# Kernel optimization log

Hardware: AMD Instinct MI355X
Metric: run time of the kernel (lower is better)

The kernel has to match this reference:

```python
import jax, jax.numpy as jnp
import numpy as np

N, T, D, K = 32, 8192, 64, 64
LOG2PI = float(np.log(2.0 * np.pi))


def setup_inputs() -> dict:
    key = jax.random.key(0)
    k1, k2, k3, k4 = jax.random.split(key, 4)
    x = jax.random.normal(k1, (N, T, D), dtype=jnp.float32)
    # valid GMM params: positive weights summing to 1, positive diagonal covariances
    weights = jax.nn.softmax(jax.random.normal(k2, (K,), dtype=jnp.float32))
    means = jax.random.normal(k3, (K, D), dtype=jnp.float32)
    covars = jax.random.uniform(k4, (K, D), dtype=jnp.float32, minval=0.5, maxval=1.5)
    return {"x": x, "weights": weights, "means": means, "covars": covars}


def _posterior(x, weights, means, covars):
    # diagonal-GMM predict_proba without materializing [N,T,K,D]:
    # sum_d (x-mu)^2/c = sum x^2/c - 2 sum x*mu/c + sum mu^2/c
    inv_c = 1.0 / covars                                   # [K,D]
    quad = (jnp.einsum('ntd,kd->ntk', x * x, inv_c)
            - 2.0 * jnp.einsum('ntd,kd->ntk', x, means * inv_c)
            + jnp.sum(means * means * inv_c, axis=-1))      # [N,T,K]
    log_prob = (jnp.log(weights)
                - 0.5 * (D * LOG2PI + jnp.sum(jnp.log(covars), axis=-1) + quad))
    return jax.nn.softmax(log_prob, axis=-1)               # [N,T,K]


def reference(x, weights, means, covars):
    # p = predict_proba * weights, renormalized over K (as in the torch code)
    p = _posterior(x, weights, means, covars) * weights
    p = p / jnp.sum(p, axis=-1, keepdims=True)             # [N,T,K]

    # pooled statistics over T (einsum avoids the [N,T,K,D] intermediate)
    s0 = jnp.sum(p, axis=1)                                # [N,K]
    s1 = jnp.einsum('ntk,ntd->nkd', p, x)                  # [N,K,D]
    s2 = jnp.einsum('ntk,ntd->nkd', p, x * x)              # [N,K,D]

    sw = jnp.sqrt(weights)                                 # [K]
    v0 = (s0 - T * weights) / sw                           # [N,K]
    v1 = (s1 - means * s0[..., None]) / (sw[:, None] * jnp.sqrt(covars))
    v2 = (s2 - 2.0 * means * s1 + (means ** 2 - covars) * s0[..., None]) / (
        jnp.sqrt(jnp.float32(2.0)) * sw[:, None] * covars)

    v = jnp.concatenate([v0[..., None], v1, v2], axis=2).reshape(x.shape[0], -1)
    # power normalization then L2 normalization
    v = jnp.sign(v) * jnp.sqrt(jnp.abs(v))
    v = v / jnp.linalg.norm(v, axis=1, keepdims=True)
    return v
```

## Files before the change

kernel.cpp:

```cpp
#include <hip/hip_runtime.h>
#include <math.h>

#define N_  32
#define T_  8192
#define D_  64
#define K_  64
#define CHUNKS 32
#define TOK_PER_BLOCK (T_ / CHUNKS)
#define TB 64
#define NBATCH (TOK_PER_BLOCK / TB)
#define STATS_PER_N (K_ + 2 * K_ * D_)
#define XSTR 72

typedef _Float16 half_t;
typedef __attribute__((ext_vector_type(8)))  _Float16 v8h;
typedef __attribute__((ext_vector_type(4)))  float    v4f;
typedef __attribute__((ext_vector_type(16))) float    v16f;

__global__ void prep_kernel(const float* __restrict__ w, const float* __restrict__ mu,
                            const float* __restrict__ cv, float* __restrict__ Ap,
                            half_t* __restrict__ WH, float* __restrict__ ssq) {
    if (blockIdx.x < 8) {
#pragma unroll
        for (int i = 0; i < 4; ++i) {
            const int e = blockIdx.x * 1024 + i * 256 + threadIdx.x;
            const int j = e & 7, l = (e >> 3) & 63, fs = e >> 9;
            const int tile = fs >> 2, s = fs & 3;
            const int kc = 16 * tile + (l & 15);
            const int f  = 32 * s + 8 * (l >> 4) + j;
            float val;
            if (f < 64) val = mu[kc * 64 + f] / cv[kc * 64 + f];
            else        val = -0.5f / cv[kc * 64 + (f - 64)];
            WH[e] = (half_t)val;
        }
    } else {
        if (threadIdx.x < 32) ssq[threadIdx.x] = 0.f;
        if (threadIdx.x < K_) {
            const int k = threadIdx.x;
            float acc = 0.f;
            for (int d = 0; d < D_; ++d) {
                const int idx = k * D_ + d;
                const float c = cv[idx], m = mu[idx];
                acc += logf(c) + m * m / c;
            }
            Ap[k] = 2.f * logf(w[k]) - 0.5f * acc;
        }
    }
}

__launch_bounds__(256, 3)
__global__ void main_kernel(const float* __restrict__ x, const float* __restrict__ Ap,
                            const half_t* __restrict__ WH, float* __restrict__ outbuf,
                            int mode) {
    __shared__ half_t Xs[TB][XSTR];
    __shared__ half_t Qs[TB][XSTR];
    __shared__ half_t Pt[K_][XSTR];
    __shared__ float  s0sh[4][64];

    const int tid  = threadIdx.x;
    const int lane = tid & 63;
    const int wv   = tid >> 6;
    const int chunk = blockIdx.x;
    const int n     = blockIdx.y;
    const int q     = lane >> 4;
    const int c0    = lane & 15;
    const int tok   = 16 * wv + c0;

    v8h Wf[16];
#pragma unroll
    for (int t = 0; t < 4; ++t)
#pragma unroll
        for (int s = 0; s < 4; ++s)
            Wf[t * 4 + s] = *(const v8h*)(WH + (size_t)((t * 4 + s) * 64 + lane) * 8);

    float apv[16];
#pragma unroll
    for (int t = 0; t < 4; ++t)
#pragma unroll
        for (int r = 0; r < 4; ++r) apv[t * 4 + r] = Ap[16 * t + 4 * q + r];

    float S0loc[16];
#pragma unroll
    for (int j = 0; j < 16; ++j) S0loc[j] = 0.f;

    const int sig = wv >> 1;
    const int dh  = wv & 1;
    v16f accB[2];
#pragma unroll
    for (int m = 0; m < 2; ++m)
#pragma unroll
        for (int r = 0; r < 16; ++r) accB[m][r] = 0.f;

    const size_t xbase = ((size_t)n * T_ + (size_t)chunk * TOK_PER_BLOCK) * (size_t)D_;
    const float* xrow0 = x + xbase + tok * 64 + 8 * q;

    float4 R[4];
    R[0] = *(const float4*)(xrow0);
    R[1] = *(const float4*)(xrow0 + 4);
    R[2] = *(const float4*)(xrow0 + 32);
    R[3] = *(const float4*)(xrow0 + 36);

#pragma unroll 1
    for (int batch = 0; batch < NBATCH; ++batch) {
        v8h xh0, xh1, qh0, qh1;
        {
            const float4 a = R[0], b = R[1], c = R[2], d = R[3];
            xh0[0] = (half_t)a.x; xh0[1] = (half_t)a.y; xh0[2] = (half_t)a.z; xh0[3] = (half_t)a.w;
            xh0[4] = (half_t)b.x; xh0[5] = (half_t)b.y; xh0[6] = (half_t)b.z; xh0[7] = (half_t)b.w;
            xh1[0] = (half_t)c.x; xh1[1] = (half_t)c.y; xh1[2] = (half_t)c.z; xh1[3] = (half_t)c.w;
            xh1[4] = (half_t)d.x; xh1[5] = (half_t)d.y; xh1[6] = (half_t)d.z; xh1[7] = (half_t)d.w;
            qh0[0] = (half_t)(a.x * a.x); qh0[1] = (half_t)(a.y * a.y);
            qh0[2] = (half_t)(a.z * a.z); qh0[3] = (half_t)(a.w * a.w);
            qh0[4] = (half_t)(b.x * b.x); qh0[5] = (half_t)(b.y * b.y);
            qh0[6] = (half_t)(b.z * b.z); qh0[7] = (half_t)(b.w * b.w);
            qh1[0] = (half_t)(c.x * c.x); qh1[1] = (half_t)(c.y * c.y);
            qh1[2] = (half_t)(c.z * c.z); qh1[3] = (half_t)(c.w * c.w);
            qh1[4] = (half_t)(d.x * d.x); qh1[5] = (half_t)(d.y * d.y);
            qh1[6] = (half_t)(d.z * d.z); qh1[7] = (half_t)(d.w * d.w);
            *(v8h*)&Xs[tok][8 * q]      = xh0;
            *(v8h*)&Xs[tok][32 + 8 * q] = xh1;
            *(v8h*)&Qs[tok][8 * q]      = qh0;
            *(v8h*)&Qs[tok][32 + 8 * q] = qh1;
        }

        if (batch + 1 < NBATCH) {
            const float* xr = xrow0 + (size_t)(batch + 1) * TB * D_;
            R[0] = *(const float4*)(xr);
            R[1] = *(const float4*)(xr + 4);
            R[2] = *(const float4*)(xr + 32);
            R[3] = *(const float4*)(xr + 36);
        }

        {
            v4f acc[4];
#pragma unroll
            for (int t = 0; t < 4; ++t) acc[t] = (v4f)(0.f);
#pragma unroll
            for (int t = 0; t < 4; ++t) {
                acc[t] = __builtin_amdgcn_mfma_f32_16x16x32_f16(Wf[t * 4 + 0], xh0, acc[t], 0, 0, 0);
                acc[t] = __builtin_amdgcn_mfma_f32_16x16x32_f16(Wf[t * 4 + 1], xh1, acc[t], 0, 0, 0);
                acc[t] = __builtin_amdgcn_mfma_f32_16x16x32_f16(Wf[t * 4 + 2], qh0, acc[t], 0, 0, 0);
                acc[t] = __builtin_amdgcn_mfma_f32_16x16x32_f16(Wf[t * 4 + 3], qh1, acc[t], 0, 0, 0);
            }
            float pv[16];
            float m = -1e30f;
#pragma unroll
            for (int t = 0; t < 4; ++t)
#pragma unroll
                for (int r = 0; r < 4; ++r) {
                    const float lg = acc[t][r] + apv[t * 4 + r];
                    pv[t * 4 + r] = lg;
                    m = fmaxf(m, lg);
                }
            m = fmaxf(m, __shfl_xor(m, 16, 64));
            m = fmaxf(m, __shfl_xor(m, 32, 64));
            float ssum = 0.f;
#pragma unroll
            for (int j = 0; j < 16; ++j) { pv[j] = __expf(pv[j] - m); ssum += pv[j]; }
            ssum += __shfl_xor(ssum, 16, 64);
            ssum += __shfl_xor(ssum, 32, 64);
            const float rs = 1.f / ssum;
#pragma unroll
            for (int j = 0; j < 16; ++j) { pv[j] *= rs; S0loc[j] += pv[j]; }
#pragma unroll
            for (int t = 0; t < 4; ++t)
#pragma unroll
                for (int r = 0; r < 4; ++r)
                    Pt[16 * t + 4 * q + r][tok] = (half_t)pv[t * 4 + r];
        }
        __syncthreads();

        {
            const half_t* Bsrc = (sig == 0) ? &Xs[0][0] : &Qs[0][0];
            const int m   = lane & 31;
            const int h   = lane >> 5;
            const int d   = 32 * dh + m;
            const half_t* Arow0 = &Pt[m][0];
            const half_t* Arow1 = &Pt[32 + m][0];
#pragma unroll
            for (int st = 0; st < 4; ++st) {
                const int tB = 16 * st + 8 * h;
                const v8h a0 = *(const v8h*)(Arow0 + tB);
                const v8h a1 = *(const v8h*)(Arow1 + tB);
                v8h bf;
#pragma unroll
                for (int j = 0; j < 8; ++j)
                    bf[j] = Bsrc[(tB + j) * XSTR + d];
                accB[0] = __builtin_amdgcn_mfma_f32_32x32x16_f16(a0, bf, accB[0], 0, 0, 0);
                accB[1] = __builtin_amdgcn_mfma_f32_32x32x16_f16(a1, bf, accB[1], 0, 0, 0);
            }
        }
        __syncthreads();
    }

#pragma unroll
    for (int j = 0; j < 16; ++j) {
        float v = S0loc[j];
        v += __shfl_xor(v, 1, 64);
        v += __shfl_xor(v, 2, 64);
        v += __shfl_xor(v, 4, 64);
        v += __shfl_xor(v, 8, 64);
        S0loc[j] = v;
    }
    if (c0 == 0) {
#pragma unroll
        for (int t = 0; t < 4; ++t)
#pragma unroll
            for (int r = 0; r < 4; ++r)
                s0sh[wv][16 * t + 4 * q + r] = S0loc[t * 4 + r];
    }
    __syncthreads();

    if (mode == 1) {
        float* dstb = outbuf + (size_t)(n * CHUNKS + chunk) * STATS_PER_N;
        if (tid < 64)
            dstb[tid] = s0sh[0][tid] + s0sh[1][tid] + s0sh[2][tid] + s0sh[3][tid];
        const int d = 32 * dh + (lane & 31);
        float* dst = dstb + 64 + sig * 4096;
#pragma unroll
        for (int mt = 0; mt < 2; ++mt)
#pragma unroll
            for (int r = 0; r < 16; ++r) {
                const int kc = 32 * mt + (r & 3) + 8 * (r >> 2) + 4 * (lane >> 5);
                dst[kc * 64 + d] = accB[mt][r];
            }
    } else {
        float* sb = outbuf + (size_t)n * STATS_PER_N;
        if (tid < 64)
            atomicAdd(&sb[tid], s0sh[0][tid] + s0sh[1][tid] + s0sh[2][tid] + s0sh[3][tid]);
        const int d = 32 * dh + (lane & 31);
        float* dst = sb + 64 + sig * 4096;
#pragma unroll
        for (int mt = 0; mt < 2; ++mt)
#pragma unroll
            for (int r = 0; r < 16; ++r) {
                const int kc = 32 * mt + (r & 3) + 8 * (r >> 2) + 4 * (lane >> 5);
                atomicAdd(&dst[kc * 64 + d], accB[mt][r]);
            }
    }
}

__global__ void reduce_pow_kernel(const float* __restrict__ partials,
                                  const float* __restrict__ w, const float* __restrict__ mu,
                                  const float* __restrict__ cv,
                                  float* __restrict__ us, float* __restrict__ ssq) {
    __shared__ float red[4];
    const int e = blockIdx.x * 256 + threadIdx.x;
    const int n = blockIdx.y;
    float u = 0.f;
    if (e < STATS_PER_N) {
        const float* base = partials + (size_t)n * CHUNKS * STATS_PER_N;
        float sv = 0.f;
#pragma unroll 8
        for (int c = 0; c < CHUNKS; ++c) sv += base[(size_t)c * STATS_PER_N + e];
        float v; int oidx;
        if (e < 64) {
            const float wv = w[e];
            v = (sv - (float)T_ * wv) * rsqrtf(wv);
            oidx = e * 129;
        } else if (e < 64 + 4096) {
            const int idx = e - 64, k = idx >> 6, d = idx & 63;
            float s0v = 0.f;
#pragma unroll 8
            for (int c = 0; c < CHUNKS; ++c) s0v += base[(size_t)c * STATS_PER_N + k];
            v = (sv - mu[idx] * s0v) * rsqrtf(w[k] * cv[idx]);
            oidx = k * 129 + 1 + d;
        } else {
            const int idx = e - 4160, k = idx >> 6, d = idx & 63;
            float s0v = 0.f, s1v = 0.f;
#pragma unroll 4
            for (int c = 0; c < CHUNKS; ++c) {
                s0v += base[(size_t)c * STATS_PER_N + k];
                s1v += base[(size_t)c * STATS_PER_N + 64 + idx];
            }
            const float m_ = mu[idx], c_ = cv[idx];
            v = (sv - 2.f * m_ * s1v + (m_ * m_ - c_) * s0v) * (rsqrtf(2.f * w[k]) / c_);
            oidx = k * 129 + 65 + d;
        }
        u = (v >= 0.f) ? sqrtf(v) : -sqrtf(-v);
        us[(size_t)n * STATS_PER_N + oidx] = u;
    }
    float ss = u * u;
#pragma unroll
    for (int off = 32; off > 0; off >>= 1) ss += __shfl_xor(ss, off, 64);
    if ((threadIdx.x & 63) == 0) red[threadIdx.x >> 6] = ss;
    __syncthreads();
    if (threadIdx.x == 0)
        atomicAdd(&ssq[n], red[0] + red[1] + red[2] + red[3]);
}

__global__ void scale_kernel(const float* __restrict__ us, const float* __restrict__ ssq,
                             float* __restrict__ out) {
    const int e = blockIdx.x * 256 + threadIdx.x;
    const int n = blockIdx.y;
    if (e < STATS_PER_N)
        out[(size_t)n * STATS_PER_N + e] = us[(size_t)n * STATS_PER_N + e] * rsqrtf(ssq[n]);
}

__global__ void fin_kernel(const float* __restrict__ w, const float* __restrict__ mu,
                           const float* __restrict__ cv, const float* __restrict__ stats,
                           float* __restrict__ out) {
    __shared__ float us[STATS_PER_N];
    __shared__ float red[4];
    const int n   = blockIdx.x;
    const int tid = threadIdx.x;
    const float* sb = stats + (size_t)n * STATS_PER_N;

    float ss = 0.f;
    if (tid < 64) {
        const float wv = w[tid];
        const float v = (sb[tid] - (float)T_ * wv) * rsqrtf(wv);
        const float u = (v >= 0.f) ? sqrtf(v) : -sqrtf(-v);
        us[tid * 129] = u;
        ss = fmaf(u, u, ss);
    }
#pragma unroll 1
    for (int i = 0; i < 16; ++i) {
        const int idx = i * 256 + tid;
        const int k = idx >> 6, d = idx & 63;
        const float v = (sb[64 + idx] - mu[idx] * sb[k]) * rsqrtf(w[k] * cv[idx]);
        const float u = (v >= 0.f) ? sqrtf(v) : -sqrtf(-v);
        us[k * 129 + 1 + d] = u;
        ss = fmaf(u, u, ss);
    }
#pragma unroll 1
    for (int i = 0; i < 16; ++i) {
        const int idx = i * 256 + tid;
        const int k = idx >> 6, d = idx & 63;
        const float m_ = mu[idx], c_ = cv[idx];
        const float s1v = sb[64 + idx], s2v = sb[64 + 4096 + idx];
        const float v = (s2v - 2.f * m_ * s1v + (m_ * m_ - c_) * sb[k]) *
                        (rsqrtf(2.f * w[k]) / c_);
        const float u = (v >= 0.f) ? sqrtf(v) : -sqrtf(-v);
        us[k * 129 + 65 + d] = u;
        ss = fmaf(u, u, ss);
    }
#pragma unroll
    for (int off = 32; off > 0; off >>= 1) ss += __shfl_xor(ss, off, 64);
    if ((tid & 63) == 0) red[tid >> 6] = ss;
    __syncthreads();
    const float tot = red[0] + red[1] + red[2] + red[3];
    const float rn = rsqrtf(tot);
    for (int e = tid; e < STATS_PER_N; e += 256)
        out[(size_t)n * STATS_PER_N + e] = us[e] * rn;
}

extern "C" void kernel_launch(void* const* d_in, const int* in_sizes, int n_in,
                              void* d_out, int out_size, void* d_ws, size_t ws_size,
                              hipStream_t stream) {
    const float* x  = (const float*)d_in[0];
    const float* w  = (const float*)d_in[1];
    const float* mu = (const float*)d_in[2];
    const float* cv = (const float*)d_in[3];
    float* out = (float*)d_out;

    const size_t part_elems = (size_t)CHUNKS * N_ * STATS_PER_N;
    const size_t us_elems   = (size_t)N_ * STATS_PER_N;
    const size_t need_big = (part_elems + us_elems + 32 + K_ + (size_t)K_ * 64) * sizeof(float);

    if (ws_size >= need_big) {
        float* partials = (float*)d_ws;
        float* us  = partials + part_elems;
        float* ssq = us + us_elems;
        float* Ap  = ssq + 32;
        half_t* WH = (half_t*)(Ap + K_);

        prep_kernel<<<9, 256, 0, stream>>>(w, mu, cv, Ap, WH, ssq);
        main_kernel<<<dim3(CHUNKS, N_), 256, 0, stream>>>(x, Ap, WH, partials, 1);
        reduce_pow_kernel<<<dim3(33, N_), 256, 0, stream>>>(partials, w, mu, cv, us, ssq);
        scale_kernel<<<dim3(33, N_), 256, 0, stream>>>(us, ssq, out);
    } else {
        float* stats = (float*)d_ws;
        float* ssq = stats + us_elems;
        float* Ap  = ssq + 32;
        half_t* WH = (half_t*)(Ap + K_);

        hipMemsetAsync(stats, 0, us_elems * sizeof(float), stream);
        prep_kernel<<<9, 256, 0, stream>>>(w, mu, cv, Ap, WH, ssq);
        main_kernel<<<dim3(CHUNKS, N_), 256, 0, stream>>>(x, Ap, WH, stats, 0);
        fin_kernel<<<N_, 256, 0, stream>>>(w, mu, cv, stats, out);
    }
}
```

Measured before the change: 154.6 us.

## Process 128-token batches per block with 16 chunks and two token groups

Halves the number of chunks per sequence so each block covers 512 tokens, and doubles the batch to 128 tokens by having each wave process two 16-token groups before each barrier pair. The goal is to cut the number of __syncthreads per token, the number of partial-stat blocks that must be reduced afterwards, and to double register prefetch depth. In exchange it uses more shared memory and registers (launch bounds drop to 2 blocks per CU) and launches fewer blocks, which may reduce occupancy and latency hiding.

```diff
diff --git a/kernel.cpp b/kernel.cpp
--- a/kernel.cpp
+++ b/kernel.cpp
@@ -5,12 +5,12 @@
 #define T_  8192
 #define D_  64
 #define K_  64
-#define CHUNKS 32
-#define TOK_PER_BLOCK (T_ / CHUNKS)
-#define TB 64
-#define NBATCH (TOK_PER_BLOCK / TB)
+#define CHUNKS 16
+#define TB 128
+#define NBATCH 4
 #define STATS_PER_N (K_ + 2 * K_ * D_)
 #define XSTR 72
+#define PSTR 136
 
 typedef _Float16 half_t;
 typedef __attribute__((ext_vector_type(8)))  _Float16 v8h;
@@ -48,13 +48,13 @@
     }
 }
 
-__launch_bounds__(256, 3)
+__launch_bounds__(256, 2)
 __global__ void main_kernel(const float* __restrict__ x, const float* __restrict__ Ap,
                             const half_t* __restrict__ WH, float* __restrict__ outbuf,
                             int mode) {
     __shared__ half_t Xs[TB][XSTR];
     __shared__ half_t Qs[TB][XSTR];
-    __shared__ half_t Pt[K_][XSTR];
+    __shared__ half_t Pt[K_][PSTR];
     __shared__ float  s0sh[4][64];
 
     const int tid  = threadIdx.x;
@@ -64,7 +64,8 @@
     const int n     = blockIdx.y;
     const int q     = lane >> 4;
     const int c0    = lane & 15;
-    const int tok   = 16 * wv + c0;
+    const int tok0  = 16 * wv + c0;
+    const int tok1  = tok0 + 64;
 
     v8h Wf[16];
 #pragma unroll
@@ -91,83 +92,88 @@
 #pragma unroll
         for (int r = 0; r < 16; ++r) accB[m][r] = 0.f;
 
-    const size_t xbase = ((size_t)n * T_ + (size_t)chunk * TOK_PER_BLOCK) * (size_t)D_;
-    const float* xrow0 = x + xbase + tok * 64 + 8 * q;
-
-    float4 R[4];
-    R[0] = *(const float4*)(xrow0);
-    R[1] = *(const float4*)(xrow0 + 4);
-    R[2] = *(const float4*)(xrow0 + 32);
-    R[3] = *(const float4*)(xrow0 + 36);
+    const size_t xbase = ((size_t)n * T_ + (size_t)chunk * (NBATCH * TB)) * (size_t)D_;
+    const float* xrow0 = x + xbase + tok0 * 64 + 8 * q;
+    const float* xrow1 = x + xbase + tok1 * 64 + 8 * q;
+
+    float4 RA[4], RB[4];
+    RA[0] = *(const float4*)(xrow0);      RA[1] = *(const float4*)(xrow0 + 4);
+    RA[2] = *(const float4*)(xrow0 + 32); RA[3] = *(const float4*)(xrow0 + 36);
+    RB[0] = *(const float4*)(xrow1);      RB[1] = *(const float4*)(xrow1 + 4);
+    RB[2] = *(const float4*)(xrow1 + 32); RB[3] = *(const float4*)(xrow1 + 36);
+
+#define PROCESS_GROUP(Rg, xrowg, tokg)                                          \
+    {                                                                           \
+        v8h xh0, xh1, qh0, qh1;                                                 \
+        {                                                                       \
+            const float4 a = Rg[0], b = Rg[1], c = Rg[2], d = Rg[3];            \
+            xh0[0] = (half_t)a.x; xh0[1] = (half_t)a.y; xh0[2] = (half_t)a.z; xh0[3] = (half_t)a.w; \
+            xh0[4] = (half_t)b.x; xh0[5] = (half_t)b.y; xh0[6] = (half_t)b.z; xh0[7] = (half_t)b.w; \
+            xh1[0] = (half_t)c.x; xh1[1] = (half_t)c.y; xh1[2] = (half_t)c.z; xh1[3] = (half_t)c.w; \
+            xh1[4] = (half_t)d.x; xh1[5] = (half_t)d.y; xh1[6] = (half_t)d.z; xh1[7] = (half_t)d.w; \
+            qh0[0] = (half_t)(a.x * a.x); qh0[1] = (half_t)(a.y * a.y);         \
+            qh0[2] = (half_t)(a.z * a.z); qh0[3] = (half_t)(a.w * a.w);         \
+            qh0[4] = (half_t)(b.x * b.x); qh0[5] = (half_t)(b.y * b.y);         \
+            qh0[6] = (half_t)(b.z * b.z); qh0[7] = (half_t)(b.w * b.w);         \
+            qh1[0] = (half_t)(c.x * c.x); qh1[1] = (half_t)(c.y * c.y);         \
+            qh1[2] = (half_t)(c.z * c.z); qh1[3] = (half_t)(c.w * c.w);         \
+            qh1[4] = (half_t)(d.x * d.x); qh1[5] = (half_t)(d.y * d.y);         \
+            qh1[6] = (half_t)(d.z * d.z); qh1[7] = (half_t)(d.w * d.w);         \
+            *(v8h*)&Xs[tokg][8 * q]      = xh0;                                 \
+            *(v8h*)&Xs[tokg][32 + 8 * q] = xh1;                                 \
+            *(v8h*)&Qs[tokg][8 * q]      = qh0;                                 \
+            *(v8h*)&Qs[tokg][32 + 8 * q] = qh1;                                 \
+        }                                                                       \
+        if (batch + 1 < NBATCH) {                                               \
+            const float* xr = xrowg + (size_t)(batch + 1) * TB * D_;            \
+            Rg[0] = *(const float4*)(xr);                                       \
+            Rg[1] = *(const float4*)(xr + 4);                                   \
+            Rg[2] = *(const float4*)(xr + 32);                                  \
+            Rg[3] = *(const float4*)(xr + 36);                                  \
+        }                                                                       \
+        {                                                                       \
+            v4f acc[4];                                                         \
+            _Pragma("unroll")                                                   \
+            for (int t = 0; t < 4; ++t) acc[t] = (v4f)(0.f);                    \
+            _Pragma("unroll")                                                   \
+            for (int t = 0; t < 4; ++t) {                                       \
+                acc[t] = __builtin_amdgcn_mfma_f32_16x16x32_f16(Wf[t * 4 + 0], xh0, acc[t], 0, 0, 0); \
+                acc[t] = __builtin_amdgcn_mfma_f32_16x16x32_f16(Wf[t * 4 + 1], xh1, acc[t], 0, 0, 0); \
+                acc[t] = __builtin_amdgcn_mfma_f32_16x16x32_f16(Wf[t * 4 + 2], qh0, acc[t], 0, 0, 0); \
+                acc[t] = __builtin_amdgcn_mfma_f32_16x16x32_f16(Wf[t * 4 + 3], qh1, acc[t], 0, 0, 0); \
+            }                                                                   \
+            float pv[16];                                                       \
+            float m = -1e30f;                                                   \
+            _Pragma("unroll")                                                   \
+            for (int t = 0; t < 4; ++t)                                         \
+                _Pragma("unroll")                                               \
+                for (int r = 0; r < 4; ++r) {                                   \
+                    const float lg = acc[t][r] + apv[t * 4 + r];                \
+                    pv[t * 4 + r] = lg;                                         \
+                    m = fmaxf(m, lg);                                           \
+                }                                                               \
+            m = fmaxf(m, __shfl_xor(m, 16, 64));                                \
+            m = fmaxf(m, __shfl_xor(m, 32, 64));                                \
+            float ssum = 0.f;                                                   \
+            _Pragma("unroll")                                                   \
+            for (int j = 0; j < 16; ++j) { pv[j] = __expf(pv[j] - m); ssum += pv[j]; } \
+            ssum += __shfl_xor(ssum, 16, 64);                                   \
+            ssum += __shfl_xor(ssum, 32, 64);                                   \
+            const float rs = 1.f / ssum;                                        \
+            _Pragma("unroll")                                                   \
+            for (int j = 0; j < 16; ++j) { pv[j] *= rs; S0loc[j] += pv[j]; }    \
+            _Pragma("unroll")                                                   \
+            for (int t = 0; t < 4; ++t)                                         \
+                _Pragma("unroll")                                               \
+                for (int r = 0; r < 4; ++r)                                     \
+                    Pt[16 * t + 4 * q + r][tokg] = (half_t)pv[t * 4 + r];       \
+        }                                                                       \
+    }
 
 #pragma unroll 1
     for (int batch = 0; batch < NBATCH; ++batch) {
-        v8h xh0, xh1, qh0, qh1;
-        {
-            const float4 a = R[0], b = R[1], c = R[2], d = R[3];
-            xh0[0] = (half_t)a.x; xh0[1] = (half_t)a.y; xh0[2] = (half_t)a.z; xh0[3] = (half_t)a.w;
-            xh0[4] = (half_t)b.x; xh0[5] = (half_t)b.y; xh0[6] = (half_t)b.z; xh0[7] = (half_t)b.w;
-            xh1[0] = (half_t)c.x; xh1[1] = (half_t)c.y; xh1[2] = (half_t)c.z; xh1[3] = (half_t)c.w;
-            xh1[4] = (half_t)d.x; xh1[5] = (half_t)d.y; xh1[6] = (half_t)d.z; xh1[7] = (half_t)d.w;
-            qh0[0] = (half_t)(a.x * a.x); qh0[1] = (half_t)(a.y * a.y);
-            qh0[2] = (half_t)(a.z * a.z); qh0[3] = (half_t)(a.w * a.w);
-            qh0[4] = (half_t)(b.x * b.x); qh0[5] = (half_t)(b.y * b.y);
-            qh0[6] = (half_t)(b.z * b.z); qh0[7] = (half_t)(b.w * b.w);
-            qh1[0] = (half_t)(c.x * c.x); qh1[1] = (half_t)(c.y * c.y);
-            qh1[2] = (half_t)(c.z * c.z); qh1[3] = (half_t)(c.w * c.w);
-            qh1[4] = (half_t)(d.x * d.x); qh1[5] = (half_t)(d.y * d.y);
-            qh1[6] = (half_t)(d.z * d.z); qh1[7] = (half_t)(d.w * d.w);
-            *(v8h*)&Xs[tok][8 * q]      = xh0;
-            *(v8h*)&Xs[tok][32 + 8 * q] = xh1;
-            *(v8h*)&Qs[tok][8 * q]      = qh0;
-            *(v8h*)&Qs[tok][32 + 8 * q] = qh1;
-        }
-
-        if (batch + 1 < NBATCH) {
-            const float* xr = xrow0 + (size_t)(batch + 1) * TB * D_;
-            R[0] = *(const float4*)(xr);
-            R[1] = *(const float4*)(xr + 4);
-            R[2] = *(const float4*)(xr + 32);
-            R[3] = *(const float4*)(xr + 36);
-        }
-
-        {
-            v4f acc[4];
-#pragma unroll
-            for (int t = 0; t < 4; ++t) acc[t] = (v4f)(0.f);
-#pragma unroll
-            for (int t = 0; t < 4; ++t) {
-                acc[t] = __builtin_amdgcn_mfma_f32_16x16x32_f16(Wf[t * 4 + 0], xh0, acc[t], 0, 0, 0);
-                acc[t] = __builtin_amdgcn_mfma_f32_16x16x32_f16(Wf[t * 4 + 1], xh1, acc[t], 0, 0, 0);
-                acc[t] = __builtin_amdgcn_mfma_f32_16x16x32_f16(Wf[t * 4 + 2], qh0, acc[t], 0, 0, 0);
-                acc[t] = __builtin_amdgcn_mfma_f32_16x16x32_f16(Wf[t * 4 + 3], qh1, acc[t], 0, 0, 0);
-            }
-            float pv[16];
-            float m = -1e30f;
-#pragma unroll
-            for (int t = 0; t < 4; ++t)
-#pragma unroll
-                for (int r = 0; r < 4; ++r) {
-                    const float lg = acc[t][r] + apv[t * 4 + r];
-                    pv[t * 4 + r] = lg;
-                    m = fmaxf(m, lg);
-                }
-            m = fmaxf(m, __shfl_xor(m, 16, 64));
-            m = fmaxf(m, __shfl_xor(m, 32, 64));
-            float ssum = 0.f;
-#pragma unroll
-            for (int j = 0; j < 16; ++j) { pv[j] = __expf(pv[j] - m); ssum += pv[j]; }
-            ssum += __shfl_xor(ssum, 16, 64);
-            ssum += __shfl_xor(ssum, 32, 64);
-            const float rs = 1.f / ssum;
-#pragma unroll
-            for (int j = 0; j < 16; ++j) { pv[j] *= rs; S0loc[j] += pv[j]; }
-#pragma unroll
-            for (int t = 0; t < 4; ++t)
-#pragma unroll
-                for (int r = 0; r < 4; ++r)
-                    Pt[16 * t + 4 * q + r][tok] = (half_t)pv[t * 4 + r];
-        }
+        PROCESS_GROUP(RA, xrow0, tok0)
+        PROCESS_GROUP(RB, xrow1, tok1)
         __syncthreads();
 
         {
@@ -178,7 +184,7 @@
             const half_t* Arow0 = &Pt[m][0];
             const half_t* Arow1 = &Pt[32 + m][0];
 #pragma unroll
-            for (int st = 0; st < 4; ++st) {
+            for (int st = 0; st < 8; ++st) {
                 const int tB = 16 * st + 8 * h;
                 const v8h a0 = *(const v8h*)(Arow0 + tB);
                 const v8h a1 = *(const v8h*)(Arow1 + tB);
@@ -192,6 +198,7 @@
         }
         __syncthreads();
     }
+#undef PROCESS_GROUP
 
 #pragma unroll
     for (int j = 0; j < 16; ++j) {
```

After: 129.0 us. -16.6%, faster.

## Enlarge token batch per block to 256 and cut chunk count to eight

Applied to the files above, without the earlier changes.

Each block now handles 1024 tokens in four 256-token batches instead of 256 tokens in four 64-token batches, so the grid shrinks from 32 to 8 chunks per sample. Every wave keeps four groups of x rows in registers and prefetches them, and the second-stage MFMA loop runs over 256 tokens per sync. This amortises the barriers and the per-block partial-statistic writes, and leaves the reduction kernel summing four times fewer partials. In exchange the grid drops to 256 blocks with occupancy hint 1, LDS use per block grows, and register pressure rises, which risks underfilling the GPU.

```diff
diff --git a/kernel.cpp b/kernel.cpp
--- a/kernel.cpp
+++ b/kernel.cpp
@@ -5,12 +5,12 @@
 #define T_  8192
 #define D_  64
 #define K_  64
-#define CHUNKS 32
-#define TOK_PER_BLOCK (T_ / CHUNKS)
-#define TB 64
-#define NBATCH (TOK_PER_BLOCK / TB)
+#define CHUNKS 8
+#define TB 256
+#define NBATCH 4
 #define STATS_PER_N (K_ + 2 * K_ * D_)
 #define XSTR 72
+#define PSTR 264
 
 typedef _Float16 half_t;
 typedef __attribute__((ext_vector_type(8)))  _Float16 v8h;
@@ -48,13 +48,13 @@
     }
 }
 
-__launch_bounds__(256, 3)
+__launch_bounds__(256, 1)
 __global__ void main_kernel(const float* __restrict__ x, const float* __restrict__ Ap,
                             const half_t* __restrict__ WH, float* __restrict__ outbuf,
                             int mode) {
     __shared__ half_t Xs[TB][XSTR];
     __shared__ half_t Qs[TB][XSTR];
-    __shared__ half_t Pt[K_][XSTR];
+    __shared__ half_t Pt[K_][PSTR];
     __shared__ float  s0sh[4][64];
 
     const int tid  = threadIdx.x;
@@ -64,7 +64,7 @@
     const int n     = blockIdx.y;
     const int q     = lane >> 4;
     const int c0    = lane & 15;
-    const int tok   = 16 * wv + c0;
+    const int tokb  = 16 * wv + c0;
 
     v8h Wf[16];
 #pragma unroll
@@ -91,82 +91,90 @@
 #pragma unroll
         for (int r = 0; r < 16; ++r) accB[m][r] = 0.f;
 
-    const size_t xbase = ((size_t)n * T_ + (size_t)chunk * TOK_PER_BLOCK) * (size_t)D_;
-    const float* xrow0 = x + xbase + tok * 64 + 8 * q;
-
-    float4 R[4];
-    R[0] = *(const float4*)(xrow0);
-    R[1] = *(const float4*)(xrow0 + 4);
-    R[2] = *(const float4*)(xrow0 + 32);
-    R[3] = *(const float4*)(xrow0 + 36);
+    const size_t xbase = ((size_t)n * T_ + (size_t)chunk * (NBATCH * TB)) * (size_t)D_;
+
+    float4 RG[4][4];
+#pragma unroll
+    for (int g = 0; g < 4; ++g) {
+        const float* xr = x + xbase + (size_t)(tokb + 64 * g) * 64 + 8 * q;
+        RG[g][0] = *(const float4*)(xr);
+        RG[g][1] = *(const float4*)(xr + 4);
+        RG[g][2] = *(const float4*)(xr + 32);
+        RG[g][3] = *(const float4*)(xr + 36);
+    }
 
 #pragma unroll 1
     for (int batch = 0; batch < NBATCH; ++batch) {
-        v8h xh0, xh1, qh0, qh1;
-        {
-            const float4 a = R[0], b = R[1], c = R[2], d = R[3];
-            xh0[0] = (half_t)a.x; xh0[1] = (half_t)a.y; xh0[2] = (half_t)a.z; xh0[3] = (half_t)a.w;
-            xh0[4] = (half_t)b.x; xh0[5] = (half_t)b.y; xh0[6] = (half_t)b.z; xh0[7] = (half_t)b.w;
-            xh1[0] = (half_t)c.x; xh1[1] = (half_t)c.y; xh1[2] = (half_t)c.z; xh1[3] = (half_t)c.w;
-            xh1[4] = (half_t)d.x; xh1[5] = (half_t)d.y; xh1[6] = (half_t)d.z; xh1[7] = (half_t)d.w;
-            qh0[0] = (half_t)(a.x * a.x); qh0[1] = (half_t)(a.y * a.y);
-            qh0[2] = (half_t)(a.z * a.z); qh0[3] = (half_t)(a.w * a.w);
-            qh0[4] = (half_t)(b.x * b.x); qh0[5] = (half_t)(b.y * b.y);
-            qh0[6] = (half_t)(b.z * b.z); qh0[7] = (half_t)(b.w * b.w);
-            qh1[0] = (half_t)(c.x * c.x); qh1[1] = (half_t)(c.y * c.y);
-            qh1[2] = (half_t)(c.z * c.z); qh1[3] = (half_t)(c.w * c.w);
-            qh1[4] = (half_t)(d.x * d.x); qh1[5] = (half_t)(d.y * d.y);
-            qh1[6] = (half_t)(d.z * d.z); qh1[7] = (half_t)(d.w * d.w);
-            *(v8h*)&Xs[tok][8 * q]      = xh0;
-            *(v8h*)&Xs[tok][32 + 8 * q] = xh1;
-            *(v8h*)&Qs[tok][8 * q]      = qh0;
-            *(v8h*)&Qs[tok][32 + 8 * q] = qh1;
-        }
-
-        if (batch + 1 < NBATCH) {
-            const float* xr = xrow0 + (size_t)(batch + 1) * TB * D_;
-            R[0] = *(const float4*)(xr);
-            R[1] = *(const float4*)(xr + 4);
-            R[2] = *(const float4*)(xr + 32);
-            R[3] = *(const float4*)(xr + 36);
-        }
-
-        {
-            v4f acc[4];
-#pragma unroll
-            for (int t = 0; t < 4; ++t) acc[t] = (v4f)(0.f);
-#pragma unroll
-            for (int t = 0; t < 4; ++t) {
-                acc[t] = __builtin_amdgcn_mfma_f32_16x16x32_f16(Wf[t * 4 + 0], xh0, acc[t], 0, 0, 0);
-                acc[t] = __builtin_amdgcn_mfma_f32_16x16x32_f16(Wf[t * 4 + 1], xh1, acc[t], 0, 0, 0);
-                acc[t] = __builtin_amdgcn_mfma_f32_16x16x32_f16(Wf[t * 4 + 2], qh0, acc[t], 0, 0, 0);
-                acc[t] = __builtin_amdgcn_mfma_f32_16x16x32_f16(Wf[t * 4 + 3], qh1, acc[t], 0, 0, 0);
-            }
-            float pv[16];
-            float m = -1e30f;
-#pragma unroll
-            for (int t = 0; t < 4; ++t)
-#pragma unroll
-                for (int r = 0; r < 4; ++r) {
-                    const float lg = acc[t][r] + apv[t * 4 + r];
-                    pv[t * 4 + r] = lg;
-                    m = fmaxf(m, lg);
+#pragma unroll
+        for (int g = 0; g < 4; ++g) {
+            const int tokg = tokb + 64 * g;
+            v8h xh0, xh1, qh0, qh1;
+            {
+                const float4 a = RG[g][0], b = RG[g][1], c = RG[g][2], d = RG[g][3];
+                xh0[0] = (half_t)a.x; xh0[1] = (half_t)a.y; xh0[2] = (half_t)a.z; xh0[3] = (half_t)a.w;
+                xh0[4] = (half_t)b.x; xh0[5] = (half_t)b.y; xh0[6] = (half_t)b.z; xh0[7] = (half_t)b.w;
+                xh1[0] = (half_t)c.x; xh1[1] = (half_t)c.y; xh1[2] = (half_t)c.z; xh1[3] = (half_t)c.w;
+                xh1[4] = (half_t)d.x; xh1[5] = (half_t)d.y; xh1[6] = (half_t)d.z; xh1[7] = (half_t)d.w;
+                qh0[0] = (half_t)(a.x * a.x); qh0[1] = (half_t)(a.y * a.y);
+                qh0[2] = (half_t)(a.z * a.z); qh0[3] = (half_t)(a.w * a.w);
+                qh0[4] = (half_t)(b.x * b.x); qh0[5] = (half_t)(b.y * b.y);
+                qh0[6] = (half_t)(b.z * b.z); qh0[7] = (half_t)(b.w * b.w);
+                qh1[0] = (half_t)(c.x * c.x); qh1[1] = (half_t)(c.y * c.y);
+                qh1[2] = (half_t)(c.z * c.z); qh1[3] = (half_t)(c.w * c.w);
+                qh1[4] = (half_t)(d.x * d.x); qh1[5] = (half_t)(d.y * d.y);
+                qh1[6] = (half_t)(d.z * d.z); qh1[7] = (half_t)(d.w * d.w);
+                *(v8h*)&Xs[tokg][8 * q]      = xh0;
+                *(v8h*)&Xs[tokg][32 + 8 * q] = xh1;
+                *(v8h*)&Qs[tokg][8 * q]      = qh0;
+                *(v8h*)&Qs[tokg][32 + 8 * q] = qh1;
+            }
+
+            if (batch + 1 < NBATCH) {
+                const float* xr = x + xbase + (size_t)(batch + 1) * TB * D_
+                                  + (size_t)(tokb + 64 * g) * 64 + 8 * q;
+                RG[g][0] = *(const float4*)(xr);
+                RG[g][1] = *(const float4*)(xr + 4);
+                RG[g][2] = *(const float4*)(xr + 32);
+                RG[g][3] = *(const float4*)(xr + 36);
+            }
+
+            {
+                v4f acc[4];
+#pragma unroll
+                for (int t = 0; t < 4; ++t) acc[t] = (v4f)(0.f);
+#pragma unroll
+                for (int t = 0; t < 4; ++t) {
+                    acc[t] = __builtin_amdgcn_mfma_f32_16x16x32_f16(Wf[t * 4 + 0], xh0, acc[t], 0, 0, 0);
+                    acc[t] = __builtin_amdgcn_mfma_f32_16x16x32_f16(Wf[t * 4 + 1], xh1, acc[t], 0, 0, 0);
+                    acc[t] = __builtin_amdgcn_mfma_f32_16x16x32_f16(Wf[t * 4 + 2], qh0, acc[t], 0, 0, 0);
+                    acc[t] = __builtin_amdgcn_mfma_f32_16x16x32_f16(Wf[t * 4 + 3], qh1, acc[t], 0, 0, 0);
                 }
-            m = fmaxf(m, __shfl_xor(m, 16, 64));
-            m = fmaxf(m, __shfl_xor(m, 32, 64));
-            float ssum = 0.f;
-#pragma unroll
-            for (int j = 0; j < 16; ++j) { pv[j] = __expf(pv[j] - m); ssum += pv[j]; }
-            ssum += __shfl_xor(ssum, 16, 64);
-            ssum += __shfl_xor(ssum, 32, 64);
-            const float rs = 1.f / ssum;
-#pragma unroll
-            for (int j = 0; j < 16; ++j) { pv[j] *= rs; S0loc[j] += pv[j]; }
-#pragma unroll
-            for (int t = 0; t < 4; ++t)
-#pragma unroll
-                for (int r = 0; r < 4; ++r)
-                    Pt[16 * t + 4 * q + r][tok] = (half_t)pv[t * 4 + r];
+                float pv[16];
+                float m = -1e30f;
+#pragma unroll
+                for (int t = 0; t < 4; ++t)
+#pragma unroll
+                    for (int r = 0; r < 4; ++r) {
+                        const float lg = acc[t][r] + apv[t * 4 + r];
+                        pv[t * 4 + r] = lg;
+                        m = fmaxf(m, lg);
+                    }
+                m = fmaxf(m, __shfl_xor(m, 16, 64));
+                m = fmaxf(m, __shfl_xor(m, 32, 64));
+                float ssum = 0.f;
+#pragma unroll
+                for (int j = 0; j < 16; ++j) { pv[j] = __expf(pv[j] - m); ssum += pv[j]; }
+                ssum += __shfl_xor(ssum, 16, 64);
+                ssum += __shfl_xor(ssum, 32, 64);
+                const float rs = 1.f / ssum;
+#pragma unroll
+                for (int j = 0; j < 16; ++j) { pv[j] *= rs; S0loc[j] += pv[j]; }
+#pragma unroll
+                for (int t = 0; t < 4; ++t)
+#pragma unroll
+                    for (int r = 0; r < 4; ++r)
+                        Pt[16 * t + 4 * q + r][tokg] = (half_t)pv[t * 4 + r];
+            }
         }
         __syncthreads();
 
@@ -178,7 +186,7 @@
             const half_t* Arow0 = &Pt[m][0];
             const half_t* Arow1 = &Pt[32 + m][0];
 #pragma unroll
-            for (int st = 0; st < 4; ++st) {
+            for (int st = 0; st < 16; ++st) {
                 const int tB = 16 * st + 8 * h;
                 const v8h a0 = *(const v8h*)(Arow0 + tB);
                 const v8h a1 = *(const v8h*)(Arow1 + tB);
@@ -251,7 +259,7 @@
     if (e < STATS_PER_N) {
         const float* base = partials + (size_t)n * CHUNKS * STATS_PER_N;
         float sv = 0.f;
-#pragma unroll 8
+#pragma unroll
         for (int c = 0; c < CHUNKS; ++c) sv += base[(size_t)c * STATS_PER_N + e];
         float v; int oidx;
         if (e < 64) {
@@ -261,14 +269,14 @@
         } else if (e < 64 + 4096) {
             const int idx = e - 64, k = idx >> 6, d = idx & 63;
             float s0v = 0.f;
-#pragma unroll 8
+#pragma unroll
             for (int c = 0; c < CHUNKS; ++c) s0v += base[(size_t)c * STATS_PER_N + k];
             v = (sv - mu[idx] * s0v) * rsqrtf(w[k] * cv[idx]);
             oidx = k * 129 + 1 + d;
         } else {
             const int idx = e - 4160, k = idx >> 6, d = idx & 63;
             float s0v = 0.f, s1v = 0.f;
-#pragma unroll 4
+#pragma unroll
             for (int c = 0; c < CHUNKS; ++c) {
                 s0v += base[(size_t)c * STATS_PER_N + k];
                 s1v += base[(size_t)c * STATS_PER_N + 64 + idx];
```

Measured after the change: 131.7 us. 1.17x faster.
